# Optimization experiments

Measured on AMD Instinct MI355X. Metric: run time of the kernel, lower is better.

## Reference

```python
import jax, jax.numpy as jnp
import numpy as np

C_IN, SEQ_LEN, N_KERNELS, KSS, KS_MAX, BATCH = 1, 512, 1000, [7, 9, 11], 11, 64


def setup_inputs() -> dict:
    rng = np.random.default_rng(0)
    ks_l, dil_l, pad_l, lout_l = [], [], [], []
    W = np.zeros((N_KERNELS, C_IN, KS_MAX), dtype=np.float32)
    for k in range(N_KERNELS):
        ks = int(rng.choice(KSS))
        d_f = 2.0 ** rng.uniform(0.0, np.log2((SEQ_LEN - 1) // (ks - 1)))
        pad = int((ks - 1) * d_f // 2) if rng.integers(2) == 1 else 0
        d = int(d_f)
        # torch passes padding=2*pad to Conv1d -> adds 2*pad on EACH side
        lout = SEQ_LEN + 4 * pad - d * (ks - 1)
        w = rng.standard_normal((1, C_IN, ks)).astype(np.float32)
        w -= w.mean()  # center like the original (global mean)
        W[k, :, :ks] = w[0]
        ks_l.append(ks); dil_l.append(d); pad_l.append(pad); lout_l.append(lout)
    dils = np.asarray(dil_l, dtype=np.int64)
    pads = np.asarray(pad_l, dtype=np.int64)
    l_out = np.asarray(lout_l, dtype=np.int32)
    max_L = int(l_out.max())
    t = np.arange(max_L)
    j = np.arange(KS_MAX)
    # raw input index for output position t, tap j of kernel k
    raw = t[None, None, :] - 2 * pads[:, None, None] + j[None, :, None] * dils[:, None, None]
    valid = (raw >= 0) & (raw < SEQ_LEN)  # zero-padding semantics
    idx = np.clip(raw, 0, SEQ_LEN - 1).astype(np.int32)
    bias = (2.0 * (rng.random(N_KERNELS) - 0.5)).astype(np.float32)
    key = jax.random.key(0)
    x = jax.random.normal(key, (BATCH, C_IN, SEQ_LEN), dtype=jnp.float32)
    return {
        "x": x,
        "weight": jnp.asarray(W),
        "bias": jnp.asarray(bias),
        "idx": jnp.asarray(idx),
        "valid": jnp.asarray(valid),
        "l_out": jnp.asarray(l_out),
    }


def _forward(x, weight, bias, idx, valid, l_out):
    B = x.shape[0]
    K, C, KS = weight.shape
    L = idx.shape[-1]
    validf = valid.astype(x.dtype)  # [K, KS, L]
    acc = jnp.zeros((B, K, L), dtype=x.dtype)
    for j in range(KS):  # fixed small tap loop; each kernel vectorized over K
        xg = x[:, :, idx[:, j, :]]  # [B, C, K, L] gather along time
        acc = acc + jnp.einsum("bckt,kc->bkt", xg, weight[:, :, j]) * validf[None, :, j, :]
    out = acc + bias[None, :, None]  # [B, K, L]
    tmask = jnp.arange(L)[None, :] < l_out[:, None]  # [K, L] valid output positions
    neg = jnp.finfo(x.dtype).min
    mx = jnp.max(jnp.where(tmask[None], out, neg), axis=-1)  # [B, K]
    ppv = jnp.sum(jnp.where(tmask[None] & (out > 0), 1.0, 0.0), axis=-1) / l_out.astype(x.dtype)[None]
    # torch interleaves [max_i, ppv_i] along dim=1
    return jnp.stack([mx, ppv], axis=-1).reshape(B, 2 * K)


def reference(x, weight, bias, idx, valid, l_out):
    return _forward(x, weight, bias, idx, valid, l_out)
```

## Files before the change

### kernel.cpp

```cpp
#include <hip/hip_runtime.h>
#include <hip/hip_fp16.h>
#include <float.h>

constexpr int KMAX  = 11;
constexpr int SEQ   = 512;
constexpr int NB    = 64;
constexpr int NBB   = 8;
constexpr int NGRP  = NB / NBB;
constexpr int KPB   = 4;
constexpr int MSTR  = 32;
constexpr int SBASE = 512;
constexpr int WSLOT = 1600;

__device__ __forceinline__ unsigned h2b(__half2 h) { unsigned u; __builtin_memcpy(&u, &h, 4); return u; }
__device__ __forceinline__ __half2  b2h(unsigned u) { __half2 h; __builtin_memcpy(&h, &u, 4); return h; }

__device__ __forceinline__ unsigned pkmax(unsigned a, unsigned b) {
    unsigned d; asm("v_pk_max_f16 %0, %1, %2" : "=v"(d) : "v"(a), "v"(b)); return d;
}
__device__ __forceinline__ unsigned pkadd(unsigned a, unsigned b) { return h2b(__hadd2(b2h(a), b2h(b))); }
__device__ __forceinline__ __half2 h2max(__half2 a, __half2 b) { return b2h(pkmax(h2b(a), h2b(b))); }
__device__ __forceinline__ unsigned pkfma_clamp(unsigned a, unsigned b, unsigned c) {
    unsigned d; asm("v_pk_fma_f16 %0, %1, %2, %3 clamp" : "=v"(d) : "v"(a), "v"(b), "v"(c)); return d;
}

template<int CTRL>
__device__ __forceinline__ unsigned dppmov(unsigned old, unsigned v) {
    return (unsigned)__builtin_amdgcn_update_dpp((int)old, (int)v, CTRL, 0xF, 0xF, false);
}
constexpr unsigned NEGINF2 = 0xFC00FC00u;

__device__ __forceinline__ unsigned dpp_redmax(unsigned x) {
    x = pkmax(x, dppmov<0xB1 >(NEGINF2, x));
    x = pkmax(x, dppmov<0x4E >(NEGINF2, x));
    x = pkmax(x, dppmov<0x141>(NEGINF2, x));
    x = pkmax(x, dppmov<0x140>(NEGINF2, x));
    x = pkmax(x, dppmov<0x142>(NEGINF2, x));
    x = pkmax(x, dppmov<0x143>(NEGINF2, x));
    return x;
}
__device__ __forceinline__ unsigned dpp_redadd(unsigned x) {
    x = pkadd(x, dppmov<0xB1 >(0u, x));
    x = pkadd(x, dppmov<0x4E >(0u, x));
    x = pkadd(x, dppmov<0x141>(0u, x));
    x = pkadd(x, dppmov<0x140>(0u, x));
    x = pkadd(x, dppmov<0x142>(0u, x));
    x = pkadd(x, dppmov<0x143>(0u, x));
    return x;
}

__global__ __launch_bounds__(256)
void prep_kernel(const float* __restrict__ x, const float* __restrict__ w,
                 const int* __restrict__ idx, int* __restrict__ meta,
                 unsigned short* __restrict__ xt, int K, int maxL)
{
    const int tid = threadIdx.x;
    if ((int)blockIdx.x >= K) {
        const int j  = ((int)blockIdx.x - K) * 256 + tid;
        const int b  = j >> 7, s4 = j & 127;
        const float4 v = reinterpret_cast<const float4*>(x)[b * (SEQ / 4) + s4];
        const int g = b >> 3, bl = b & 7;
        unsigned short* dst = xt + ((size_t)g * SEQ + s4 * 4) * NBB + bl;
        __half h;
        h = __float2half_rn(v.x); __builtin_memcpy(&dst[0 * NBB], &h, 2);
        h = __float2half_rn(v.y); __builtin_memcpy(&dst[1 * NBB], &h, 2);
        h = __float2half_rn(v.z); __builtin_memcpy(&dst[2 * NBB], &h, 2);
        h = __float2half_rn(v.w); __builtin_memcpy(&dst[3 * NBB], &h, 2);
        return;
    }

    __shared__ int c_sh[KMAX];
    const int k = blockIdx.x, wave = tid >> 6, lane = tid & 63;

    for (int j = wave; j < KMAX; j += 4) {
        const int* row = idx + ((size_t)k * KMAX + j) * (size_t)maxL;
        int c = 0;
        for (int base = 0; base < maxL; base += 64) {
            const int t = base + lane;
            const int v = (t < maxL) ? row[t] : 0;
            const bool interior = (v > 0) && (v < SEQ - 1);
            const unsigned long long mb = __ballot(interior);
            if (mb != 0ull) {
                const int fl = __builtin_ctzll(mb);
                c = __shfl(v, fl) - (base + fl);
                break;
            }
        }
        if (lane == 0) c_sh[j] = c;
    }
    __syncthreads();

    if (tid == 0) {
        int* mk = meta + (size_t)k * MSTR;
        int n = 0;
        for (int j = 0; j < KMAX; ++j) {
            const float wj = w[(size_t)k * KMAX + j];
            if (wj != 0.0f) {
                mk[1 + n] = c_sh[j];
                __half hw = __float2half_rn(wj);
                unsigned short ub; __builtin_memcpy(&ub, &hw, 2);
                mk[12 + n] = (unsigned)ub | ((unsigned)ub << 16);
                ++n;
            }
        }
        for (int jj = n; jj < KMAX; ++jj) { mk[1 + jj] = 0; mk[12 + jj] = 0; }
        mk[0] = n;
    }
}

template<int NJ>
__device__ __forceinline__ void conv_wave(
    const char* __restrict__ xsc, int mrow, int lout, int lane, unsigned ctermb,
    unsigned (&um)[4], unsigned (&uc)[4])
{
    const __half2 zero2 = __float2half2_rn(0.f);
    const __half2 nbig2 = __float2half2_rn(-65504.f);
    const unsigned C4b  = 0x74007400u;

    int addr[NJ]; __half2 wr[NJ];
#pragma unroll
    for (int j = 0; j < NJ; ++j) {
        const int c = __builtin_amdgcn_readlane(mrow, 1 + j);
        wr[j]   = b2h((unsigned)__builtin_amdgcn_readlane(mrow, 12 + j));
        addr[j] = (lane + c + SBASE) * 16;
    }
    __half2 mx2[4], ct2[4];
#pragma unroll
    for (int m = 0; m < 4; ++m) { mx2[m] = nbig2; ct2[m] = zero2; }

    const int nfull = lout >> 6;
    const int ng4   = nfull >> 2;

    for (int g = 0; g < ng4; ++g) {
#pragma unroll
        for (int u = 0; u < 4; ++u) {
            uint4 d[NJ];
#pragma unroll
            for (int j = 0; j < NJ; ++j)
                d[j] = *reinterpret_cast<const uint4*>(xsc + addr[j] + u * 1024);
            __half2 a[4] = {zero2, zero2, zero2, zero2};
#pragma unroll
            for (int j = 0; j < NJ; ++j) {
                a[0] = __hfma2(wr[j], b2h(d[j].x), a[0]);
                a[1] = __hfma2(wr[j], b2h(d[j].y), a[1]);
                a[2] = __hfma2(wr[j], b2h(d[j].z), a[2]);
                a[3] = __hfma2(wr[j], b2h(d[j].w), a[3]);
            }
#pragma unroll
            for (int m = 0; m < 4; ++m) {
                mx2[m] = h2max(mx2[m], a[m]);
                ct2[m] = b2h(pkadd(h2b(ct2[m]), pkfma_clamp(h2b(a[m]), C4b, ctermb)));
            }
        }
#pragma unroll
        for (int j = 0; j < NJ; ++j) addr[j] += 4096;
    }
    for (int u = 0; u < (nfull & 3); ++u) {
        uint4 d[NJ];
#pragma unroll
        for (int j = 0; j < NJ; ++j)
            d[j] = *reinterpret_cast<const uint4*>(xsc + addr[j]);
        __half2 a[4] = {zero2, zero2, zero2, zero2};
#pragma unroll
        for (int j = 0; j < NJ; ++j) {
            a[0] = __hfma2(wr[j], b2h(d[j].x), a[0]);
            a[1] = __hfma2(wr[j], b2h(d[j].y), a[1]);
            a[2] = __hfma2(wr[j], b2h(d[j].z), a[2]);
            a[3] = __hfma2(wr[j], b2h(d[j].w), a[3]);
        }
#pragma unroll
        for (int m = 0; m < 4; ++m) {
            mx2[m] = h2max(mx2[m], a[m]);
            ct2[m] = b2h(pkadd(h2b(ct2[m]), pkfma_clamp(h2b(a[m]), C4b, ctermb)));
        }
#pragma unroll
        for (int j = 0; j < NJ; ++j) addr[j] += 1024;
    }
    const int rem = lout & 63;
    if (rem) {
        uint4 d[NJ];
#pragma unroll
        for (int j = 0; j < NJ; ++j)
            d[j] = *reinterpret_cast<const uint4*>(xsc + addr[j]);
        __half2 a[4] = {zero2, zero2, zero2, zero2};
#pragma unroll
        for (int j = 0; j < NJ; ++j) {
            a[0] = __hfma2(wr[j], b2h(d[j].x), a[0]);
            a[1] = __hfma2(wr[j], b2h(d[j].y), a[1]);
            a[2] = __hfma2(wr[j], b2h(d[j].z), a[2]);
            a[3] = __hfma2(wr[j], b2h(d[j].w), a[3]);
        }
        const bool tm = lane < rem;
#pragma unroll
        for (int m = 0; m < 4; ++m) {
            a[m] = tm ? a[m] : nbig2;
            mx2[m] = h2max(mx2[m], a[m]);
            ct2[m] = b2h(pkadd(h2b(ct2[m]), pkfma_clamp(h2b(a[m]), C4b, ctermb)));
        }
    }

#pragma unroll
    for (int m = 0; m < 4; ++m) {
        um[m] = dpp_redmax(h2b(mx2[m]));
        uc[m] = dpp_redadd(h2b(ct2[m]));
    }
}

__global__ __launch_bounds__(256, 4)
void rocket_main(const unsigned short* __restrict__ xt, const int* __restrict__ meta,
                 const float* __restrict__ bias, const int* __restrict__ l_out,
                 float* __restrict__ out, int K)
{
    __shared__ __align__(16) unsigned xs_u[WSLOT * 4];

    const int kbase = (int)blockIdx.x * KPB;
    const int grp   = blockIdx.y;
    const int tid   = threadIdx.x;
    const int wave  = tid >> 6, lane = tid & 63;

    const int k  = kbase + wave;
    const int kc = min(k, K - 1);
    const int   mrow_v = meta[(size_t)kc * MSTR + (lane & 31)];
    const int   lout_v = l_out[kc];
    const float bias_v = bias[kc];

    float4* xs4 = reinterpret_cast<float4*>(xs_u);
    const float4* src = reinterpret_cast<const float4*>(xt + (size_t)grp * SEQ * NBB);
    const float4 z4 = make_float4(0.f, 0.f, 0.f, 0.f);
    for (int i = tid; i < WSLOT; i += 256) {
        const int s = i - SBASE;
        xs4[i] = ((unsigned)s < (unsigned)SEQ) ? src[s] : z4;
    }
    __syncthreads();

    if (k >= K) return;

    const int nj    = __builtin_amdgcn_readlane(mrow_v, 0);
    const int lout  = __builtin_amdgcn_readfirstlane(lout_v);
    const float biasf = __int_as_float(__builtin_amdgcn_readfirstlane(__float_as_int(bias_v)));
    const unsigned ctermb = h2b(__float2half2_rn(biasf * 16384.f));

    unsigned um[4], uc[4];
    const char* xsc = reinterpret_cast<const char*>(xs_u);
    if (nj <= 7)      conv_wave<7 >(xsc, mrow_v, lout, lane, ctermb, um, uc);
    else if (nj <= 9) conv_wave<9 >(xsc, mrow_v, lout, lane, ctermb, um, uc);
    else              conv_wave<11>(xsc, mrow_v, lout, lane, ctermb, um, uc);

    if (lane == 63) {
        const float loutf = (float)lout;
#pragma unroll
        for (int m = 0; m < 4; ++m) {
            const __half2 hm = b2h(um[m]);
            const __half2 hc = b2h(uc[m]);
            float* o0 = out + (size_t)(grp * NBB + 2 * m) * (2 * K) + 2 * k;
            o0[0] = __low2float(hm) + biasf;
            o0[1] = __low2float(hc) / loutf;
            float* o1 = o0 + 2 * K;
            o1[0] = __high2float(hm) + biasf;
            o1[1] = __high2float(hc) / loutf;
        }
    }
}

extern "C" void kernel_launch(void* const* d_in, const int* in_sizes, int n_in,
                              void* d_out, int out_size, void* d_ws, size_t ws_size,
                              hipStream_t stream)
{
    const float* x    = (const float*)d_in[0];
    const float* w    = (const float*)d_in[1];
    const float* bias = (const float*)d_in[2];
    const int*   idx  = (const int*)d_in[3];
    const int*   lout = (const int*)d_in[5];
    float* out = (float*)d_out;

    const int K    = in_sizes[2];
    const int maxL = in_sizes[3] / (K * KMAX);

    int* meta = (int*)d_ws;
    size_t meta_bytes = ((size_t)K * MSTR * sizeof(int) + 255) & ~(size_t)255;
    unsigned short* xt = (unsigned short*)((char*)d_ws + meta_bytes);

    prep_kernel<<<K + 32, 256, 0, stream>>>(x, w, idx, meta, xt, K, maxL);
    rocket_main<<<dim3((K + KPB - 1) / KPB, NGRP), 256, 0, stream>>>(xt, meta, bias, lout, out, K);
}
```

Before: 30.73 us.

## Fuse prep kernel into main conv kernel, computing per-kernel metadata in-wave

Removes the separate prep launch: each block now converts its batch group's fp32 input to fp16 directly into shared memory, and each wave derives its own tap offsets from idx and packed weights from w using ballots and shuffles. The goal is to eliminate one kernel launch and the global round-trip through the workspace. In exchange, every one of the 8 batch-group blocks repeats the idx scan and input conversion for its kernels, and each wave issues 44 idx loads up front, which adds registers.

```diff
diff --git a/kernel.cpp b/kernel.cpp
--- a/kernel.cpp
+++ b/kernel.cpp
@@ -8,7 +8,6 @@
 constexpr int NBB   = 8;
 constexpr int NGRP  = NB / NBB;
 constexpr int KPB   = 4;
-constexpr int MSTR  = 32;
 constexpr int SBASE = 512;
 constexpr int WSLOT = 1600;
 
@@ -49,65 +48,6 @@
     return x;
 }
 
-__global__ __launch_bounds__(256)
-void prep_kernel(const float* __restrict__ x, const float* __restrict__ w,
-                 const int* __restrict__ idx, int* __restrict__ meta,
-                 unsigned short* __restrict__ xt, int K, int maxL)
-{
-    const int tid = threadIdx.x;
-    if ((int)blockIdx.x >= K) {
-        const int j  = ((int)blockIdx.x - K) * 256 + tid;
-        const int b  = j >> 7, s4 = j & 127;
-        const float4 v = reinterpret_cast<const float4*>(x)[b * (SEQ / 4) + s4];
-        const int g = b >> 3, bl = b & 7;
-        unsigned short* dst = xt + ((size_t)g * SEQ + s4 * 4) * NBB + bl;
-        __half h;
-        h = __float2half_rn(v.x); __builtin_memcpy(&dst[0 * NBB], &h, 2);
-        h = __float2half_rn(v.y); __builtin_memcpy(&dst[1 * NBB], &h, 2);
-        h = __float2half_rn(v.z); __builtin_memcpy(&dst[2 * NBB], &h, 2);
-        h = __float2half_rn(v.w); __builtin_memcpy(&dst[3 * NBB], &h, 2);
-        return;
-    }
-
-    __shared__ int c_sh[KMAX];
-    const int k = blockIdx.x, wave = tid >> 6, lane = tid & 63;
-
-    for (int j = wave; j < KMAX; j += 4) {
-        const int* row = idx + ((size_t)k * KMAX + j) * (size_t)maxL;
-        int c = 0;
-        for (int base = 0; base < maxL; base += 64) {
-            const int t = base + lane;
-            const int v = (t < maxL) ? row[t] : 0;
-            const bool interior = (v > 0) && (v < SEQ - 1);
-            const unsigned long long mb = __ballot(interior);
-            if (mb != 0ull) {
-                const int fl = __builtin_ctzll(mb);
-                c = __shfl(v, fl) - (base + fl);
-                break;
-            }
-        }
-        if (lane == 0) c_sh[j] = c;
-    }
-    __syncthreads();
-
-    if (tid == 0) {
-        int* mk = meta + (size_t)k * MSTR;
-        int n = 0;
-        for (int j = 0; j < KMAX; ++j) {
-            const float wj = w[(size_t)k * KMAX + j];
-            if (wj != 0.0f) {
-                mk[1 + n] = c_sh[j];
-                __half hw = __float2half_rn(wj);
-                unsigned short ub; __builtin_memcpy(&ub, &hw, 2);
-                mk[12 + n] = (unsigned)ub | ((unsigned)ub << 16);
-                ++n;
-            }
-        }
-        for (int jj = n; jj < KMAX; ++jj) { mk[1 + jj] = 0; mk[12 + jj] = 0; }
-        mk[0] = n;
-    }
-}
-
 template<int NJ>
 __device__ __forceinline__ void conv_wave(
     const char* __restrict__ xsc, int mrow, int lout, int lane, unsigned ctermb,
@@ -207,9 +147,10 @@
 }
 
 __global__ __launch_bounds__(256, 4)
-void rocket_main(const unsigned short* __restrict__ xt, const int* __restrict__ meta,
-                 const float* __restrict__ bias, const int* __restrict__ l_out,
-                 float* __restrict__ out, int K)
+void rocket_fused(const float* __restrict__ x, const float* __restrict__ w,
+                  const int* __restrict__ idx, const float* __restrict__ bias,
+                  const int* __restrict__ l_out, float* __restrict__ out,
+                  int K, int maxL)
 {
     __shared__ __align__(16) unsigned xs_u[WSLOT * 4];
 
@@ -220,39 +161,113 @@
 
     const int k  = kbase + wave;
     const int kc = min(k, K - 1);
-    const int   mrow_v = meta[(size_t)kc * MSTR + (lane & 31)];
+
+    int tr[4];
+#pragma unroll
+    for (int r = 0; r < 4; ++r) tr[r] = min(r * 64 + lane, maxL - 1);
+    const int* idk = idx + (size_t)kc * KMAX * (size_t)maxL;
+    int vv[KMAX][4];
+#pragma unroll
+    for (int j = 0; j < KMAX; ++j)
+#pragma unroll
+        for (int r = 0; r < 4; ++r)
+            vv[j][r] = idk[(size_t)j * maxL + tr[r]];
+
     const int   lout_v = l_out[kc];
     const float bias_v = bias[kc];
-
-    float4* xs4 = reinterpret_cast<float4*>(xs_u);
-    const float4* src = reinterpret_cast<const float4*>(xt + (size_t)grp * SEQ * NBB);
-    const float4 z4 = make_float4(0.f, 0.f, 0.f, 0.f);
+    const float wj_v   = (lane < KMAX) ? w[(size_t)kc * KMAX + lane] : 0.f;
+
+    uint4* xs4 = reinterpret_cast<uint4*>(xs_u);
+    const float* xg = x + (size_t)(grp * NBB) * SEQ;
     for (int i = tid; i < WSLOT; i += 256) {
         const int s = i - SBASE;
-        xs4[i] = ((unsigned)s < (unsigned)SEQ) ? src[s] : z4;
+        if ((unsigned)s >= (unsigned)SEQ) xs4[i] = make_uint4(0u, 0u, 0u, 0u);
+    }
+#pragma unroll
+    for (int h = 0; h < 2; ++h) {
+        const int s = tid + h * 256;
+        float f[8];
+#pragma unroll
+        for (int bl = 0; bl < 8; ++bl) f[bl] = xg[bl * SEQ + s];
+        unsigned p[4];
+#pragma unroll
+        for (int q = 0; q < 4; ++q)
+            p[q] = h2b(__halves2half2(__float2half_rn(f[2 * q]), __float2half_rn(f[2 * q + 1])));
+        xs4[SBASE + s] = make_uint4(p[0], p[1], p[2], p[3]);
     }
     __syncthreads();
 
     if (k >= K) return;
 
-    const int nj    = __builtin_amdgcn_readlane(mrow_v, 0);
+    int cj_lane = 0;
+#pragma unroll
+    for (int j = 0; j < KMAX; ++j) {
+        bool found = false; int cjv = 0;
+#pragma unroll
+        for (int r = 0; r < 4; ++r) {
+            const bool in = (vv[j][r] > 0) && (vv[j][r] < SEQ - 1);
+            const unsigned long long mb = __ballot(in);
+            if (!found && mb != 0ull) {
+                const int fl = __builtin_ctzll(mb);
+                const int tf = min(r * 64 + fl, maxL - 1);
+                cjv = __shfl(vv[j][r], fl) - tf;
+                found = true;
+            }
+        }
+        if (!found) {
+            for (int base = 256; base < maxL; base += 64) {
+                const int t = base + lane;
+                const int v = (t < maxL) ? idk[(size_t)j * maxL + t] : 0;
+                const bool in = (v > 0) && (v < SEQ - 1);
+                const unsigned long long mb = __ballot(in);
+                if (mb != 0ull) {
+                    const int fl = __builtin_ctzll(mb);
+                    cjv = __shfl(v, fl) - (base + fl);
+                    break;
+                }
+            }
+        }
+        cj_lane = (lane == j) ? cjv : cj_lane;
+    }
+
+    unsigned wlb;
+    { __half hw = __float2half_rn(wj_v); unsigned short ub;
+      __builtin_memcpy(&ub, &hw, 2); wlb = (unsigned)ub | ((unsigned)ub << 16); }
+    const unsigned long long nz = __ballot((lane < KMAX) && (wj_v != 0.f));
+    const int nj = (int)__popcll(nz);
+
+    int sel = 0;
+    if (lane >= 1 && lane <= KMAX) sel = lane - 1;
+    else if (lane >= 12 && lane <= 11 + KMAX) sel = lane - 12;
+    unsigned long long m = nz;
+#pragma unroll
+    for (int it = 0; it < KMAX; ++it) m = (it < sel) ? (m & (m - 1)) : m;
+    const bool vali = (m != 0ull);
+    const int ji = vali ? (int)__builtin_ctzll(m) : 0;
+    const int cv = __shfl(cj_lane, ji);
+    const int wv = __shfl((int)wlb, ji);
+    int mrow = 0;
+    if (lane == 0)               mrow = nj;
+    else if (lane <= KMAX)       mrow = vali ? cv : 0;
+    else if (lane <= 11 + KMAX)  mrow = vali ? (int)wv : 0;
+
     const int lout  = __builtin_amdgcn_readfirstlane(lout_v);
     const float biasf = __int_as_float(__builtin_amdgcn_readfirstlane(__float_as_int(bias_v)));
     const unsigned ctermb = h2b(__float2half2_rn(biasf * 16384.f));
 
     unsigned um[4], uc[4];
     const char* xsc = reinterpret_cast<const char*>(xs_u);
-    if (nj <= 7)      conv_wave<7 >(xsc, mrow_v, lout, lane, ctermb, um, uc);
-    else if (nj <= 9) conv_wave<9 >(xsc, mrow_v, lout, lane, ctermb, um, uc);
-    else              conv_wave<11>(xsc, mrow_v, lout, lane, ctermb, um, uc);
+    if (nj <= 7)      conv_wave<7 >(xsc, mrow, lout, lane, ctermb, um, uc);
+    else if (nj <= 9) conv_wave<9 >(xsc, mrow, lout, lane, ctermb, um, uc);
+    else              conv_wave<11>(xsc, mrow, lout, lane, ctermb, um, uc);
 
     if (lane == 63) {
         const float loutf = (float)lout;
 #pragma unroll
-        for (int m = 0; m < 4; ++m) {
-            const __half2 hm = b2h(um[m]);
-            const __half2 hc = b2h(uc[m]);
-            float* o0 = out + (size_t)(grp * NBB + 2 * m) * (2 * K) + 2 * k;
+        for (int m2 = 0; m2 < 4; ++m2) {
+            const __half2 hm = b2h(um[m2]);
+            const __half2 hc = b2h(uc[m2]);
+            float* o0 = out + (size_t)(grp * NBB + 2 * m2) * (2 * K) + 2 * k;
             o0[0] = __low2float(hm) + biasf;
             o0[1] = __low2float(hc) / loutf;
             float* o1 = o0 + 2 * K;
@@ -276,10 +291,6 @@
     const int K    = in_sizes[2];
     const int maxL = in_sizes[3] / (K * KMAX);
 
-    int* meta = (int*)d_ws;
-    size_t meta_bytes = ((size_t)K * MSTR * sizeof(int) + 255) & ~(size_t)255;
-    unsigned short* xt = (unsigned short*)((char*)d_ws + meta_bytes);
-
-    prep_kernel<<<K + 32, 256, 0, stream>>>(x, w, idx, meta, xt, K, maxL);
-    rocket_main<<<dim3((K + KPB - 1) / KPB, NGRP), 256, 0, stream>>>(xt, meta, bias, lout, out, K);
-}
+    rocket_fused<<<dim3((K + KPB - 1) / KPB, NGRP), 256, 0, stream>>>(
+        x, w, idx, bias, lout, out, K, maxL);
+}
```

Measured after the change: 37.69 us. 1.23x slower.
